# Performance work log

Measured on AMD Instinct MI355X. Metric: run time of the kernel, lower is better.

Reference implementation:

```python
import jax, jax.numpy as jnp
import numpy as np

B, T, V, D, H, L = 64, 256, 65, 384, 6, 6
HD = D // H
FF = 4 * D
EPS = 1e-5


def _layernorm(x, w, b):
    m = x.mean(-1, keepdims=True)
    v = ((x - m) ** 2).mean(-1, keepdims=True)
    return (x - m) / jnp.sqrt(v + EPS) * w + b


def setup_inputs() -> dict:
    key = jax.random.key(0)
    ks = jax.random.split(key, 20)
    s = lambda k, shape, scale=0.02: jax.random.normal(k, shape, dtype=jnp.float32) * scale
    inp = {
        'idx': jax.random.randint(ks[0], (B, T), 0, V),
        'tok_emb': s(ks[1], (V, D)),
        'pos_emb': s(ks[2], (T, D)),
        'ln1_w': jnp.ones((L, D), jnp.float32),
        'ln1_b': jnp.zeros((L, D), jnp.float32),
        'wq': s(ks[3], (L, H, D, HD)),
        'wk': s(ks[4], (L, H, D, HD)),
        'wv': s(ks[5], (L, H, D, HD)),
        'proj_w': s(ks[6], (L, D, D)),
        'proj_b': jnp.zeros((L, D), jnp.float32),
        'ln2_w': jnp.ones((L, D), jnp.float32),
        'ln2_b': jnp.zeros((L, D), jnp.float32),
        'ff_w1': s(ks[7], (L, D, FF)),
        'ff_b1': jnp.zeros((L, FF), jnp.float32),
        'ff_w2': s(ks[8], (L, FF, D)),
        'ff_b2': jnp.zeros((L, D), jnp.float32),
        'lnf_w': jnp.ones((D,), jnp.float32),
        'lnf_b': jnp.zeros((D,), jnp.float32),
        'head_w': s(ks[9], (D, V)),
        'head_b': jnp.zeros((V,), jnp.float32),
    }
    return inp


def reference(idx, tok_emb, pos_emb, ln1_w, ln1_b, wq, wk, wv, proj_w, proj_b,
              ln2_w, ln2_b, ff_w1, ff_b1, ff_w2, ff_b2, lnf_w, lnf_b, head_w, head_b):
    t = idx.shape[1]
    x = tok_emb[idx] + pos_emb[:t]  # [B,T,D]
    causal = jnp.tril(jnp.ones((t, t), bool))
    scale = D ** -0.5  # NOTE: original scales by n_embd**-0.5, not head_size
    for l in range(L):
        h = _layernorm(x, ln1_w[l], ln1_b[l])
        q = jnp.einsum('btd,hde->bhte', h, wq[l])
        k = jnp.einsum('btd,hde->bhte', h, wk[l])
        v = jnp.einsum('btd,hde->bhte', h, wv[l])
        wei = jnp.einsum('bhte,bhse->bhts', q, k) * scale
        wei = jnp.where(causal, wei, -jnp.inf)
        wei = jax.nn.softmax(wei, axis=-1)
        o = jnp.einsum('bhts,bhse->bhte', wei, v)
        o = o.transpose(0, 2, 1, 3).reshape(x.shape[0], t, D)  # concat heads
        x = x + o @ proj_w[l] + proj_b[l]
        h2 = _layernorm(x, ln2_w[l], ln2_b[l])
        x = x + jnp.maximum(h2 @ ff_w1[l] + ff_b1[l], 0.0) @ ff_w2[l] + ff_b2[l]
    x = _layernorm(x, lnf_w, lnf_b)
    logits = x @ head_w + head_b  # [B,T,V]
    return logits
```

## Files before the change

kernel.cpp:

```cpp
#include <hip/hip_runtime.h>
#include <hip/hip_bf16.h>
#include <math.h>

#define BB   64
#define TT   256
#define VV   65
#define DD   384
#define HH   6
#define HDD  64
#define LL   6
#define FFD  1536
#define BT   (BB * TT)
#define EPSL 1e-5f
#define SCALE 0.05103103630798287f

using bf16x8 = __attribute__((ext_vector_type(8))) short;
using f32x4  = __attribute__((ext_vector_type(4))) float;

__device__ __forceinline__ short f2bf(float f) {
    __hip_bfloat16 h = __float2bfloat16(f);
    return *reinterpret_cast<short*>(&h);
}

__device__ __forceinline__ void load_lds16(const void* g, void* lds_base) {
    __builtin_amdgcn_global_load_lds(
        (const __attribute__((address_space(1))) void*)g,
        (__attribute__((address_space(3))) void*)lds_base,
        16, 0, 0);
}

__global__ __launch_bounds__(256) void embed_k(const int* __restrict__ idx,
                                               const float* __restrict__ tok,
                                               const float* __restrict__ pos,
                                               float* __restrict__ x) {
    int i = blockIdx.x * 256 + threadIdx.x;
    int bt = i / 96;
    int d4 = i - bt * 96;
    int t  = bt & (TT - 1);
    float4 a = ((const float4*)tok)[(size_t)idx[bt] * 96 + d4];
    float4 p = ((const float4*)pos)[(size_t)t * 96 + d4];
    float4 o;
    o.x = a.x + p.x; o.y = a.y + p.y; o.z = a.z + p.z; o.w = a.w + p.w;
    ((float4*)x)[i] = o;
}

__global__ __launch_bounds__(256) void ln_k(const float* __restrict__ in,
                                            const float* __restrict__ w,
                                            const float* __restrict__ b,
                                            short* __restrict__ out) {
    int row  = blockIdx.x * 4 + (threadIdx.x >> 6);
    int lane = threadIdx.x & 63;
    const float* p = in + (size_t)row * DD;
    float vals[6];
    float s = 0.f;
#pragma unroll
    for (int j = 0; j < 6; ++j) { vals[j] = p[lane + 64 * j]; s += vals[j]; }
#pragma unroll
    for (int off = 32; off; off >>= 1) s += __shfl_xor(s, off);
    float mean = s * (1.0f / DD);
    float s2 = 0.f;
#pragma unroll
    for (int j = 0; j < 6; ++j) { float d = vals[j] - mean; s2 += d * d; }
#pragma unroll
    for (int off = 32; off; off >>= 1) s2 += __shfl_xor(s2, off);
    float rstd = rsqrtf(s2 * (1.0f / DD) + EPSL);
    short* po = out + (size_t)row * DD;
#pragma unroll
    for (int j = 0; j < 6; ++j) {
        int c = lane + 64 * j;
        po[c] = f2bf((vals[j] - mean) * rstd * w[c] + b[c]);
    }
}

__global__ __launch_bounds__(256) void wconv_k(const float* __restrict__ W,
                                               short* __restrict__ Wt,
                                               int K, int N, int Npad) {
    __shared__ float tile[32][33];
    W  += (size_t)blockIdx.z * K * N;
    Wt += (size_t)blockIdx.z * Npad * K;
    const int t  = threadIdx.x;
    const int c  = t & 31;
    const int r8 = t >> 5;
    const int k0 = blockIdx.y * 32;
    const int n0 = blockIdx.x * 32;
#pragma unroll
    for (int p = 0; p < 4; ++p) {
        int kk = r8 + 8 * p;
        int n  = n0 + c;
        tile[kk][c] = (n < N) ? W[(size_t)(k0 + kk) * N + n] : 0.f;
    }
    __syncthreads();
#pragma unroll
    for (int p = 0; p < 4; ++p) {
        int nl = r8 + 8 * p;
        Wt[(size_t)(n0 + nl) * K + k0 + c] = f2bf(tile[c][nl]);
    }
}

__global__ __launch_bounds__(256) void qkvconv_k(const float* __restrict__ wq,
                                                 const float* __restrict__ wk,
                                                 const float* __restrict__ wv,
                                                 short* __restrict__ Wt) {
    int tid = blockIdx.x * 256 + threadIdx.x;
    int e  = tid & 63;
    int k  = (tid >> 6) % 384;
    int r2 = (tid >> 6) / 384;
    int h  = r2 % 6;
    int r3 = r2 / 6;
    int part = r3 % 3;
    int l  = r3 / 3;
    const float* src = (part == 0) ? wq : (part == 1) ? wk : wv;
    float v = src[(((size_t)l * 6 + h) * 384 + k) * 64 + e];
    Wt[((size_t)l * 1152 + part * 384 + h * 64 + e) * 384 + k] = f2bf(v);
}

__global__ __launch_bounds__(512, 4) void gemm8_k(
    const short* __restrict__ A,
    const short* __restrict__ Bt,
    const float* __restrict__ bias,
    const float* __restrict__ res,
    float* __restrict__ out32,
    short* __restrict__ out16,
    int M, int K, int ldC, int ld16, int Nmax, int relu) {
    __shared__ short As[2][8192];
    __shared__ short Bs[2][8192];
    const int t  = threadIdx.x;
    const int w  = t >> 6;
    const int l  = t & 63;

    const int gx  = gridDim.x;
    const int nwg = gx * gridDim.y;
    const int lin = blockIdx.y * gx + blockIdx.x;
    const int cpx = nwg >> 3;
    const int swz = (lin & 7) * cpx + (lin >> 3);
    const int m0 = (swz / gx) * 128;
    const int n0 = (swz % gx) * 128;

    const int wr = w >> 2, wc = w & 3;
    const int fr = l & 15, fq = l >> 4;

    int srow[2], scol[2];
#pragma unroll
    for (int qi = 0; qi < 2; ++qi) {
        int S = (w * 2 + qi) * 1024 + l * 16;
        int r = S >> 7;
        int c = (S >> 4) & 7;
        srow[qi] = r;
        scol[qi] = c ^ (r & 7);
    }

    f32x4 acc[4][2];
#pragma unroll
    for (int i = 0; i < 4; ++i)
#pragma unroll
        for (int j = 0; j < 2; ++j) acc[i][j] = (f32x4)(0.0f);

    const int nt = K >> 6;
    int cur = 0;

#pragma unroll
    for (int qi = 0; qi < 2; ++qi) {
        load_lds16(A + (size_t)(m0 + srow[qi]) * K + scol[qi] * 8,
                   (char*)As[0] + (w * 2 + qi) * 1024);
        load_lds16(Bt + (size_t)(n0 + srow[qi]) * K + scol[qi] * 8,
                   (char*)Bs[0] + (w * 2 + qi) * 1024);
    }
    asm volatile("s_waitcnt vmcnt(0)" ::: "memory");
    __syncthreads();

    for (int tk = 0; tk < nt; ++tk) {
        const int k1 = (tk + 1) << 6;
        if (tk + 1 < nt) {
#pragma unroll
            for (int qi = 0; qi < 2; ++qi) {
                load_lds16(A + (size_t)(m0 + srow[qi]) * K + k1 + scol[qi] * 8,
                           (char*)As[cur ^ 1] + (w * 2 + qi) * 1024);
                load_lds16(Bt + (size_t)(n0 + srow[qi]) * K + k1 + scol[qi] * 8,
                           (char*)Bs[cur ^ 1] + (w * 2 + qi) * 1024);
            }
        }
        const char* Ab = (const char*)As[cur];
        const char* Bb = (const char*)Bs[cur];
#pragma unroll
        for (int ks = 0; ks < 2; ++ks) {
            const int kc = ks * 4 + fq;
            bf16x8 af[4], bfv[2];
#pragma unroll
            for (int mf = 0; mf < 4; ++mf) {
                int ar = wr * 64 + mf * 16 + fr;
                af[mf] = *reinterpret_cast<const bf16x8*>(
                    Ab + ar * 128 + ((kc ^ (ar & 7)) << 4));
            }
#pragma unroll
            for (int nf = 0; nf < 2; ++nf) {
                int br = wc * 32 + nf * 16 + fr;
                bfv[nf] = *reinterpret_cast<const bf16x8*>(
                    Bb + br * 128 + ((kc ^ (br & 7)) << 4));
            }
#pragma unroll
            for (int mf = 0; mf < 4; ++mf)
#pragma unroll
                for (int nf = 0; nf < 2; ++nf)
                    acc[mf][nf] = __builtin_amdgcn_mfma_f32_16x16x32_bf16(
                        af[mf], bfv[nf], acc[mf][nf], 0, 0, 0);
        }
        if (tk + 1 < nt) {
            asm volatile("s_waitcnt vmcnt(0)" ::: "memory");
            __syncthreads();
            cur ^= 1;
        }
    }

#pragma unroll
    for (int mf = 0; mf < 4; ++mf) {
#pragma unroll
        for (int nf = 0; nf < 2; ++nf) {
            int n = n0 + wc * 32 + nf * 16 + fr;
            if (n < Nmax) {
#pragma unroll
                for (int j = 0; j < 4; ++j) {
                    int m = m0 + wr * 64 + mf * 16 + fq * 4 + j;
                    float v = acc[mf][nf][j];
                    if (bias)  v += bias[n];
                    if (res)   v += res[(size_t)m * ldC + n];
                    if (relu)  v = fmaxf(v, 0.f);
                    if (out32) out32[(size_t)m * ldC + n] = v;
                    if (out16) out16[(size_t)m * ld16 + n] = f2bf(v);
                }
            }
        }
    }
}

__global__ __launch_bounds__(256) void attn_mfma_k(const short* __restrict__ qkv,
                                                   short* __restrict__ o) {
    __shared__ short Vt[16384];
    __shared__ short Pw[4][4096];

    const int hh = blockIdx.x;
    const int bb = blockIdx.y;
    const int t  = threadIdx.x;
    const int w  = t >> 6;
    const int lane = t & 63;
    const int fr = lane & 15, fq = lane >> 4;
    const int bt0 = bb * TT;

    {
        const int r0 = (t & 127) * 2;
        const int dbase = (t >> 7) * 32;
        const short* v0 = qkv + (size_t)(bt0 + r0) * 1152 + 768 + hh * 64 + dbase;
        short a0[32], a1[32];
#pragma unroll
        for (int i = 0; i < 4; ++i) {
            *(bf16x8*)(a0 + i * 8) = *(const bf16x8*)(v0 + i * 8);
            *(bf16x8*)(a1 + i * 8) = *(const bf16x8*)(v0 + 1152 + i * 8);
        }
#pragma unroll
        for (int i = 0; i < 32; ++i) {
            int d = dbase + i;
            int byte = (d * 512 + r0 * 2) ^ ((d & 7) << 4);
            unsigned int pk = (unsigned int)(unsigned short)a0[i] |
                              ((unsigned int)(unsigned short)a1[i] << 16);
            *(unsigned int*)((char*)Vt + byte) = pk;
        }
    }
    __syncthreads();

    char* PwW = (char*)Pw[w];

    bf16x8 qb[4][2];
#pragma unroll
    for (int nf = 0; nf < 4; ++nf)
#pragma unroll
        for (int ks = 0; ks < 2; ++ks)
            qb[nf][ks] = *(const bf16x8*)(qkv + (size_t)(bt0 + w * 64 + nf * 16 + fr) * 1152 +
                                          hh * 64 + ks * 32 + fq * 8);

    f32x4 o_acc[4][4];
#pragma unroll
    for (int i = 0; i < 4; ++i)
#pragma unroll
        for (int j = 0; j < 4; ++j) o_acc[i][j] = (f32x4)(0.0f);
    float m_run[4], l_run[4];
#pragma unroll
    for (int nf = 0; nf < 4; ++nf) { m_run[nf] = -1e30f; l_run[nf] = 0.f; }

    for (int kt = 0; kt <= w; ++kt) {
        bf16x8 ak[4][2];
#pragma unroll
        for (int mf = 0; mf < 4; ++mf)
#pragma unroll
            for (int ks = 0; ks < 2; ++ks)
                ak[mf][ks] = *(const bf16x8*)(qkv + (size_t)(bt0 + kt * 64 + mf * 16 + fr) * 1152 +
                                              384 + hh * 64 + ks * 32 + fq * 8);

        f32x4 s[4][4];
#pragma unroll
        for (int i = 0; i < 4; ++i)
#pragma unroll
            for (int j = 0; j < 4; ++j) s[i][j] = (f32x4)(0.0f);
#pragma unroll
        for (int ks = 0; ks < 2; ++ks)
#pragma unroll
            for (int mf = 0; mf < 4; ++mf)
#pragma unroll
                for (int nf = 0; nf < 4; ++nf)
                    s[mf][nf] = __builtin_amdgcn_mfma_f32_16x16x32_bf16(
                        ak[mf][ks], qb[nf][ks], s[mf][nf], 0, 0, 0);

        const bool diag = (kt == w);
#pragma unroll
        for (int mf = 0; mf < 4; ++mf)
#pragma unroll
            for (int nf = 0; nf < 4; ++nf)
#pragma unroll
                for (int j = 0; j < 4; ++j) {
                    float v = s[mf][nf][j] * SCALE;
                    if (diag && (mf * 16 + fq * 4 + j > nf * 16 + fr)) v = -1e30f;
                    s[mf][nf][j] = v;
                }

        float fac[4];
#pragma unroll
        for (int nf = 0; nf < 4; ++nf) {
            float mx = -1e30f;
#pragma unroll
            for (int mf = 0; mf < 4; ++mf)
#pragma unroll
                for (int j = 0; j < 4; ++j) mx = fmaxf(mx, s[mf][nf][j]);
            mx = fmaxf(mx, __shfl_xor(mx, 16));
            mx = fmaxf(mx, __shfl_xor(mx, 32));
            float mnew = fmaxf(m_run[nf], mx);
            fac[nf] = __expf(m_run[nf] - mnew);
            m_run[nf] = mnew;
        }

#pragma unroll
        for (int nf = 0; nf < 4; ++nf) {
            float ps = 0.f;
#pragma unroll
            for (int mf = 0; mf < 4; ++mf)
#pragma unroll
                for (int j = 0; j < 4; ++j) {
                    float p = __expf(s[mf][nf][j] - m_run[nf]);
                    s[mf][nf][j] = p;
                    ps += p;
                }
            ps += __shfl_xor(ps, 16);
            ps += __shfl_xor(ps, 32);
            l_run[nf] = l_run[nf] * fac[nf] + ps;
        }

#pragma unroll
        for (int mf = 0; mf < 4; ++mf)
#pragma unroll
            for (int nf = 0; nf < 4; ++nf) {
                unsigned long long pk =
                    (unsigned long long)(unsigned short)f2bf(s[mf][nf][0]) |
                    ((unsigned long long)(unsigned short)f2bf(s[mf][nf][1]) << 16) |
                    ((unsigned long long)(unsigned short)f2bf(s[mf][nf][2]) << 32) |
                    ((unsigned long long)(unsigned short)f2bf(s[mf][nf][3]) << 48);
                int q = nf * 16 + fr;
                int byte = (q * 128 + mf * 32 + fq * 8) ^ ((q & 7) << 4);
                *(unsigned long long*)(PwW + byte) = pk;
            }

#pragma unroll
        for (int j = 0; j < 4; ++j) {
            int src = (lane & 48) + ((lane & 48) >> 2) + j;
#pragma unroll
            for (int mo = 0; mo < 4; ++mo) {
                float f = __shfl(fac[mo], src);
#pragma unroll
                for (int df = 0; df < 4; ++df) o_acc[mo][df][j] *= f;
            }
        }

        bf16x8 ap[4][2], bv[4][2];
#pragma unroll
        for (int mo = 0; mo < 4; ++mo)
#pragma unroll
            for (int ks = 0; ks < 2; ++ks) {
                int byte = ((mo * 16 + fr) * 128 + ks * 64 + fq * 16) ^ ((fr & 7) << 4);
                ap[mo][ks] = *(const bf16x8*)(PwW + byte);
            }
#pragma unroll
        for (int df = 0; df < 4; ++df)
#pragma unroll
            for (int ks = 0; ks < 2; ++ks) {
                int byte = ((df * 16 + fr) * 512 + kt * 128 + ks * 64 + fq * 16) ^ ((fr & 7) << 4);
                bv[df][ks] = *(const bf16x8*)((const char*)Vt + byte);
            }
#pragma unroll
        for (int ks = 0; ks < 2; ++ks)
#pragma unroll
            for (int mo = 0; mo < 4; ++mo)
#pragma unroll
                for (int df = 0; df < 4; ++df)
                    o_acc[mo][df] = __builtin_amdgcn_mfma_f32_16x16x32_bf16(
                        ap[mo][ks], bv[df][ks], o_acc[mo][df], 0, 0, 0);
    }

    float linv[4];
#pragma unroll
    for (int nf = 0; nf < 4; ++nf) linv[nf] = 1.0f / l_run[nf];
#pragma unroll
    for (int j = 0; j < 4; ++j) {
        int src = (lane & 48) + ((lane & 48) >> 2) + j;
#pragma unroll
        for (int mo = 0; mo < 4; ++mo) {
            float li = __shfl(linv[mo], src);
#pragma unroll
            for (int df = 0; df < 4; ++df) {
                float val = o_acc[mo][df][j] * li;
                o[(size_t)(bt0 + w * 64 + mo * 16 + fq * 4 + j) * DD + hh * 64 + df * 16 + fr] =
                    f2bf(val);
            }
        }
    }
}

extern "C" void kernel_launch(void* const* d_in, const int* in_sizes, int n_in,
                              void* d_out, int out_size, void* d_ws, size_t ws_size,
                              hipStream_t stream) {
    const int*   idx     = (const int*)d_in[0];
    const float* tok_emb = (const float*)d_in[1];
    const float* pos_emb = (const float*)d_in[2];
    const float* ln1_w   = (const float*)d_in[3];
    const float* ln1_b   = (const float*)d_in[4];
    const float* wq      = (const float*)d_in[5];
    const float* wk      = (const float*)d_in[6];
    const float* wv      = (const float*)d_in[7];
    const float* proj_w  = (const float*)d_in[8];
    const float* proj_b  = (const float*)d_in[9];
    const float* ln2_w   = (const float*)d_in[10];
    const float* ln2_b   = (const float*)d_in[11];
    const float* ff_w1   = (const float*)d_in[12];
    const float* ff_b1   = (const float*)d_in[13];
    const float* ff_w2   = (const float*)d_in[14];
    const float* ff_b2   = (const float*)d_in[15];
    const float* lnf_w   = (const float*)d_in[16];
    const float* lnf_b   = (const float*)d_in[17];
    const float* head_w  = (const float*)d_in[18];
    const float* head_b  = (const float*)d_in[19];
    float* out = (float*)d_out;

    char* p = (char*)d_ws;
    float* x      = (float*)p;  p += (size_t)BT * DD * 4;
    short* qkv16  = (short*)p;  p += (size_t)BT * 1152 * 2;
    short* h16    = (short*)p;  p += (size_t)BT * DD * 2;
    short* o16    = (short*)p;  p += (size_t)BT * DD * 2;
    short* ff16   = (short*)p;  p += (size_t)BT * FFD * 2;
    short* wqkvT  = (short*)p;  p += (size_t)LL * 1152 * 384 * 2;
    short* projT  = (short*)p;  p += (size_t)LL * 384 * 384 * 2;
    short* ff1T   = (short*)p;  p += (size_t)LL * 1536 * 384 * 2;
    short* ff2T   = (short*)p;  p += (size_t)LL * 384 * 1536 * 2;
    short* headT  = (short*)p;  p += (size_t)128 * 384 * 2;

    const dim3 blk(256);
    const dim3 blk512(512);

    qkvconv_k<<<dim3(2654208 / 256), blk, 0, stream>>>(wq, wk, wv, wqkvT);
    wconv_k<<<dim3(12, 12, 6), blk, 0, stream>>>(proj_w, projT, 384, 384, 384);
    wconv_k<<<dim3(48, 12, 6), blk, 0, stream>>>(ff_w1, ff1T, 384, 1536, 1536);
    wconv_k<<<dim3(12, 48, 6), blk, 0, stream>>>(ff_w2, ff2T, 1536, 384, 384);
    wconv_k<<<dim3(4, 12, 1), blk, 0, stream>>>(head_w, headT, 384, 65, 128);

    embed_k<<<dim3((BT * 96) / 256), blk, 0, stream>>>(idx, tok_emb, pos_emb, x);

    const dim3 gLN(BT / 4);
    const dim3 gAttn(HH, BB);
    const dim3 gQKV(1152 / 128, BT / 128);
    const dim3 gD(384 / 128, BT / 128);
    const dim3 gFF(1536 / 128, BT / 128);
    const dim3 gHead(1, BT / 128);

    for (int l = 0; l < LL; ++l) {
        const size_t dOff = (size_t)l * DD;

        ln_k<<<gLN, blk, 0, stream>>>(x, ln1_w + dOff, ln1_b + dOff, h16);

        gemm8_k<<<gQKV, blk512, 0, stream>>>(h16, wqkvT + (size_t)l * 1152 * 384,
                                             nullptr, nullptr, nullptr, qkv16,
                                             BT, 384, 1152, 1152, 1152, 0);

        attn_mfma_k<<<gAttn, blk, 0, stream>>>(qkv16, o16);

        gemm8_k<<<gD, blk512, 0, stream>>>(o16, projT + (size_t)l * 384 * 384,
                                           proj_b + dOff, x, x, nullptr,
                                           BT, 384, 384, 0, 384, 0);

        ln_k<<<gLN, blk, 0, stream>>>(x, ln2_w + dOff, ln2_b + dOff, h16);

        gemm8_k<<<gFF, blk512, 0, stream>>>(h16, ff1T + (size_t)l * 1536 * 384,
                                            ff_b1 + (size_t)l * FFD, nullptr,
                                            nullptr, ff16,
                                            BT, 384, 1536, 1536, 1536, 1);

        gemm8_k<<<gD, blk512, 0, stream>>>(ff16, ff2T + (size_t)l * 384 * 1536,
                                           ff_b2 + dOff, x, x, nullptr,
                                           BT, 1536, 384, 0, 384, 0);
    }

    ln_k<<<gLN, blk, 0, stream>>>(x, lnf_w, lnf_b, h16);
    gemm8_k<<<gHead, blk512, 0, stream>>>(h16, headT, head_b, nullptr, out, nullptr,
                                          BT, 384, 65, 0, 65, 0);
}
```

Measured before the change: 1.368 ms.

## Replace LDS-staged GEMM with direct global-to-register fragment loads

The GEMM no longer stages A and B tiles through shared memory with global_load_lds and barriers. Each wave now loads its MFMA fragments straight from global memory into registers, double-buffered across two k-tiles. This removes LDS traffic and __syncthreads, but loses cross-wave reuse: each A row is fetched by 4 waves and each B row by 2, so global/L2 traffic rises, and the loads are 16-byte strided per row rather than fully coalesced. Register pressure also rises, and the occupancy hint in launch_bounds is dropped.

```diff
diff --git a/kernel.cpp b/kernel.cpp
--- a/kernel.cpp
+++ b/kernel.cpp
@@ -20,13 +20,6 @@
 __device__ __forceinline__ short f2bf(float f) {
     __hip_bfloat16 h = __float2bfloat16(f);
     return *reinterpret_cast<short*>(&h);
-}
-
-__device__ __forceinline__ void load_lds16(const void* g, void* lds_base) {
-    __builtin_amdgcn_global_load_lds(
-        (const __attribute__((address_space(1))) void*)g,
-        (__attribute__((address_space(3))) void*)lds_base,
-        16, 0, 0);
 }
 
 __global__ __launch_bounds__(256) void embed_k(const int* __restrict__ idx,
@@ -114,7 +107,7 @@
     Wt[((size_t)l * 1152 + part * 384 + h * 64 + e) * 384 + k] = f2bf(v);
 }
 
-__global__ __launch_bounds__(512, 4) void gemm8_k(
+__global__ __launch_bounds__(512) void gemmreg_k(
     const short* __restrict__ A,
     const short* __restrict__ Bt,
     const float* __restrict__ bias,
@@ -122,8 +115,6 @@
     float* __restrict__ out32,
     short* __restrict__ out16,
     int M, int K, int ldC, int ld16, int Nmax, int relu) {
-    __shared__ short As[2][8192];
-    __shared__ short Bs[2][8192];
     const int t  = threadIdx.x;
     const int w  = t >> 6;
     const int l  = t & 63;
@@ -139,15 +130,14 @@
     const int wr = w >> 2, wc = w & 3;
     const int fr = l & 15, fq = l >> 4;
 
-    int srow[2], scol[2];
-#pragma unroll
-    for (int qi = 0; qi < 2; ++qi) {
-        int S = (w * 2 + qi) * 1024 + l * 16;
-        int r = S >> 7;
-        int c = (S >> 4) & 7;
-        srow[qi] = r;
-        scol[qi] = c ^ (r & 7);
-    }
+    const short* Ap[4];
+#pragma unroll
+    for (int mf = 0; mf < 4; ++mf)
+        Ap[mf] = A + (size_t)(m0 + wr * 64 + mf * 16 + fr) * K + fq * 8;
+    const short* Bp[2];
+#pragma unroll
+    for (int nf = 0; nf < 2; ++nf)
+        Bp[nf] = Bt + (size_t)(n0 + wc * 32 + nf * 16 + fr) * K + fq * 8;
 
     f32x4 acc[4][2];
 #pragma unroll
@@ -156,59 +146,64 @@
         for (int j = 0; j < 2; ++j) acc[i][j] = (f32x4)(0.0f);
 
     const int nt = K >> 6;
-    int cur = 0;
-
-#pragma unroll
-    for (int qi = 0; qi < 2; ++qi) {
-        load_lds16(A + (size_t)(m0 + srow[qi]) * K + scol[qi] * 8,
-                   (char*)As[0] + (w * 2 + qi) * 1024);
-        load_lds16(Bt + (size_t)(n0 + srow[qi]) * K + scol[qi] * 8,
-                   (char*)Bs[0] + (w * 2 + qi) * 1024);
-    }
-    asm volatile("s_waitcnt vmcnt(0)" ::: "memory");
-    __syncthreads();
-
-    for (int tk = 0; tk < nt; ++tk) {
-        const int k1 = (tk + 1) << 6;
-        if (tk + 1 < nt) {
-#pragma unroll
-            for (int qi = 0; qi < 2; ++qi) {
-                load_lds16(A + (size_t)(m0 + srow[qi]) * K + k1 + scol[qi] * 8,
-                           (char*)As[cur ^ 1] + (w * 2 + qi) * 1024);
-                load_lds16(Bt + (size_t)(n0 + srow[qi]) * K + k1 + scol[qi] * 8,
-                           (char*)Bs[cur ^ 1] + (w * 2 + qi) * 1024);
-            }
-        }
-        const char* Ab = (const char*)As[cur];
-        const char* Bb = (const char*)Bs[cur];
-#pragma unroll
-        for (int ks = 0; ks < 2; ++ks) {
-            const int kc = ks * 4 + fq;
-            bf16x8 af[4], bfv[2];
-#pragma unroll
-            for (int mf = 0; mf < 4; ++mf) {
-                int ar = wr * 64 + mf * 16 + fr;
-                af[mf] = *reinterpret_cast<const bf16x8*>(
-                    Ab + ar * 128 + ((kc ^ (ar & 7)) << 4));
-            }
-#pragma unroll
-            for (int nf = 0; nf < 2; ++nf) {
-                int br = wc * 32 + nf * 16 + fr;
-                bfv[nf] = *reinterpret_cast<const bf16x8*>(
-                    Bb + br * 128 + ((kc ^ (br & 7)) << 4));
-            }
+
+    bf16x8 a0[4][2], b0[2][2], a1[4][2], b1[2][2];
+
+#pragma unroll
+    for (int mf = 0; mf < 4; ++mf)
+#pragma unroll
+        for (int ks = 0; ks < 2; ++ks)
+            a0[mf][ks] = *(const bf16x8*)(Ap[mf] + ks * 32);
+#pragma unroll
+    for (int nf = 0; nf < 2; ++nf)
+#pragma unroll
+        for (int ks = 0; ks < 2; ++ks)
+            b0[nf][ks] = *(const bf16x8*)(Bp[nf] + ks * 32);
+
+    for (int tk = 0; tk < nt; tk += 2) {
+        const int kb = (tk + 1) << 6;
+#pragma unroll
+        for (int mf = 0; mf < 4; ++mf)
+#pragma unroll
+            for (int ks = 0; ks < 2; ++ks)
+                a1[mf][ks] = *(const bf16x8*)(Ap[mf] + kb + ks * 32);
+#pragma unroll
+        for (int nf = 0; nf < 2; ++nf)
+#pragma unroll
+            for (int ks = 0; ks < 2; ++ks)
+                b1[nf][ks] = *(const bf16x8*)(Bp[nf] + kb + ks * 32);
+
+#pragma unroll
+        for (int ks = 0; ks < 2; ++ks)
 #pragma unroll
             for (int mf = 0; mf < 4; ++mf)
 #pragma unroll
                 for (int nf = 0; nf < 2; ++nf)
                     acc[mf][nf] = __builtin_amdgcn_mfma_f32_16x16x32_bf16(
-                        af[mf], bfv[nf], acc[mf][nf], 0, 0, 0);
-        }
-        if (tk + 1 < nt) {
-            asm volatile("s_waitcnt vmcnt(0)" ::: "memory");
-            __syncthreads();
-            cur ^= 1;
-        }
+                        a0[mf][ks], b0[nf][ks], acc[mf][nf], 0, 0, 0);
+
+        if (tk + 2 < nt) {
+            const int kc = (tk + 2) << 6;
+#pragma unroll
+            for (int mf = 0; mf < 4; ++mf)
+#pragma unroll
+                for (int ks = 0; ks < 2; ++ks)
+                    a0[mf][ks] = *(const bf16x8*)(Ap[mf] + kc + ks * 32);
+#pragma unroll
+            for (int nf = 0; nf < 2; ++nf)
+#pragma unroll
+                for (int ks = 0; ks < 2; ++ks)
+                    b0[nf][ks] = *(const bf16x8*)(Bp[nf] + kc + ks * 32);
+        }
+
+#pragma unroll
+        for (int ks = 0; ks < 2; ++ks)
+#pragma unroll
+            for (int mf = 0; mf < 4; ++mf)
+#pragma unroll
+                for (int nf = 0; nf < 2; ++nf)
+                    acc[mf][nf] = __builtin_amdgcn_mfma_f32_16x16x32_bf16(
+                        a1[mf][ks], b1[nf][ks], acc[mf][nf], 0, 0, 0);
     }
 
 #pragma unroll
@@ -480,29 +475,29 @@
 
         ln_k<<<gLN, blk, 0, stream>>>(x, ln1_w + dOff, ln1_b + dOff, h16);
 
-        gemm8_k<<<gQKV, blk512, 0, stream>>>(h16, wqkvT + (size_t)l * 1152 * 384,
-                                             nullptr, nullptr, nullptr, qkv16,
-                                             BT, 384, 1152, 1152, 1152, 0);
+        gemmreg_k<<<gQKV, blk512, 0, stream>>>(h16, wqkvT + (size_t)l * 1152 * 384,
+                                               nullptr, nullptr, nullptr, qkv16,
+                                               BT, 384, 1152, 1152, 1152, 0);
 
         attn_mfma_k<<<gAttn, blk, 0, stream>>>(qkv16, o16);
 
-        gemm8_k<<<gD, blk512, 0, stream>>>(o16, projT + (size_t)l * 384 * 384,
-                                           proj_b + dOff, x, x, nullptr,
-                                           BT, 384, 384, 0, 384, 0);
+        gemmreg_k<<<gD, blk512, 0, stream>>>(o16, projT + (size_t)l * 384 * 384,
+                                             proj_b + dOff, x, x, nullptr,
+                                             BT, 384, 384, 0, 384, 0);
 
         ln_k<<<gLN, blk, 0, stream>>>(x, ln2_w + dOff, ln2_b + dOff, h16);
 
-        gemm8_k<<<gFF, blk512, 0, stream>>>(h16, ff1T + (size_t)l * 1536 * 384,
-                                            ff_b1 + (size_t)l * FFD, nullptr,
-                                            nullptr, ff16,
-                                            BT, 384, 1536, 1536, 1536, 1);
-
-        gemm8_k<<<gD, blk512, 0, stream>>>(ff16, ff2T + (size_t)l * 384 * 1536,
-                                           ff_b2 + dOff, x, x, nullptr,
-                                           BT, 1536, 384, 0, 384, 0);
+        gemmreg_k<<<gFF, blk512, 0, stream>>>(h16, ff1T + (size_t)l * 1536 * 384,
+                                              ff_b1 + (size_t)l * FFD, nullptr,
+                                              nullptr, ff16,
+                                              BT, 384, 1536, 1536, 1536, 1);
+
+        gemmreg_k<<<gD, blk512, 0, stream>>>(ff16, ff2T + (size_t)l * 384 * 1536,
+                                             ff_b2 + dOff, x, x, nullptr,
+                                             BT, 1536, 384, 0, 384, 0);
     }
 
     ln_k<<<gLN, blk, 0, stream>>>(x, lnf_w, lnf_b, h16);
-    gemm8_k<<<gHead, blk512, 0, stream>>>(h16, headT, head_b, nullptr, out, nullptr,
-                                          BT, 384, 65, 0, 65, 0);
-}
+    gemmreg_k<<<gHead, blk512, 0, stream>>>(h16, headT, head_b, nullptr, out, nullptr,
+                                            BT, 384, 65, 0, 65, 0);
+}
```

Measured after the change: 3.124 ms. 128% more time.

## Switch GEMMs to 64x64 tiles with single-buffered LDS and more blocks

Applied to the files above, without the earlier changes.

Replaces the 128x128, 512-thread double-buffered GEMM with a 64x64, 256-thread single-buffered kernel. Grids grow fourfold so each launch has more workgroups across the CUs, and the kernel adds s_setprio around the MFMA section. The trade is the loss of global-load/compute overlap from double buffering, and lower operand reuse per tile, which means more global traffic.

```diff
diff --git a/kernel.cpp b/kernel.cpp
--- a/kernel.cpp
+++ b/kernel.cpp
@@ -114,7 +114,7 @@
     Wt[((size_t)l * 1152 + part * 384 + h * 64 + e) * 384 + k] = f2bf(v);
 }
 
-__global__ __launch_bounds__(512, 4) void gemm8_k(
+__global__ __launch_bounds__(256, 8) void gemm64_k(
     const short* __restrict__ A,
     const short* __restrict__ Bt,
     const float* __restrict__ bias,
@@ -122,8 +122,8 @@
     float* __restrict__ out32,
     short* __restrict__ out16,
     int M, int K, int ldC, int ld16, int Nmax, int relu) {
-    __shared__ short As[2][8192];
-    __shared__ short Bs[2][8192];
+    __shared__ short As[4096];
+    __shared__ short Bs[4096];
     const int t  = threadIdx.x;
     const int w  = t >> 6;
     const int l  = t & 63;
@@ -133,93 +133,82 @@
     const int lin = blockIdx.y * gx + blockIdx.x;
     const int cpx = nwg >> 3;
     const int swz = (lin & 7) * cpx + (lin >> 3);
-    const int m0 = (swz / gx) * 128;
-    const int n0 = (swz % gx) * 128;
-
-    const int wr = w >> 2, wc = w & 3;
+    const int m0 = (swz / gx) * 64;
+    const int n0 = (swz % gx) * 64;
+
+    const int wr = w >> 1, wc = w & 1;
     const int fr = l & 15, fq = l >> 4;
 
     int srow[2], scol[2];
 #pragma unroll
     for (int qi = 0; qi < 2; ++qi) {
-        int S = (w * 2 + qi) * 1024 + l * 16;
-        int r = S >> 7;
-        int c = (S >> 4) & 7;
+        int s = w * 2 + qi;
+        int r = s * 8 + (l >> 3);
+        int c = l & 7;
         srow[qi] = r;
         scol[qi] = c ^ (r & 7);
     }
 
-    f32x4 acc[4][2];
-#pragma unroll
-    for (int i = 0; i < 4; ++i)
+    f32x4 acc[2][2];
+#pragma unroll
+    for (int i = 0; i < 2; ++i)
 #pragma unroll
         for (int j = 0; j < 2; ++j) acc[i][j] = (f32x4)(0.0f);
 
     const int nt = K >> 6;
-    int cur = 0;
-
-#pragma unroll
-    for (int qi = 0; qi < 2; ++qi) {
-        load_lds16(A + (size_t)(m0 + srow[qi]) * K + scol[qi] * 8,
-                   (char*)As[0] + (w * 2 + qi) * 1024);
-        load_lds16(Bt + (size_t)(n0 + srow[qi]) * K + scol[qi] * 8,
-                   (char*)Bs[0] + (w * 2 + qi) * 1024);
-    }
-    asm volatile("s_waitcnt vmcnt(0)" ::: "memory");
-    __syncthreads();
 
     for (int tk = 0; tk < nt; ++tk) {
-        const int k1 = (tk + 1) << 6;
-        if (tk + 1 < nt) {
-#pragma unroll
-            for (int qi = 0; qi < 2; ++qi) {
-                load_lds16(A + (size_t)(m0 + srow[qi]) * K + k1 + scol[qi] * 8,
-                           (char*)As[cur ^ 1] + (w * 2 + qi) * 1024);
-                load_lds16(Bt + (size_t)(n0 + srow[qi]) * K + k1 + scol[qi] * 8,
-                           (char*)Bs[cur ^ 1] + (w * 2 + qi) * 1024);
-            }
-        }
-        const char* Ab = (const char*)As[cur];
-        const char* Bb = (const char*)Bs[cur];
+        const int k0 = tk << 6;
+#pragma unroll
+        for (int qi = 0; qi < 2; ++qi) {
+            load_lds16(A + (size_t)(m0 + srow[qi]) * K + k0 + scol[qi] * 8,
+                       (char*)As + (w * 2 + qi) * 1024);
+        }
+#pragma unroll
+        for (int qi = 0; qi < 2; ++qi) {
+            load_lds16(Bt + (size_t)(n0 + srow[qi]) * K + k0 + scol[qi] * 8,
+                       (char*)Bs + (w * 2 + qi) * 1024);
+        }
+        asm volatile("s_waitcnt vmcnt(0)" ::: "memory");
+        __syncthreads();
+
+        __builtin_amdgcn_s_setprio(1);
 #pragma unroll
         for (int ks = 0; ks < 2; ++ks) {
             const int kc = ks * 4 + fq;
-            bf16x8 af[4], bfv[2];
-#pragma unroll
-            for (int mf = 0; mf < 4; ++mf) {
-                int ar = wr * 64 + mf * 16 + fr;
+            bf16x8 af[2], bfv[2];
+#pragma unroll
+            for (int mf = 0; mf < 2; ++mf) {
+                int ar = wr * 32 + mf * 16 + fr;
                 af[mf] = *reinterpret_cast<const bf16x8*>(
-                    Ab + ar * 128 + ((kc ^ (ar & 7)) << 4));
+                    (const char*)As + ar * 128 + ((kc ^ (ar & 7)) << 4));
             }
 #pragma unroll
             for (int nf = 0; nf < 2; ++nf) {
                 int br = wc * 32 + nf * 16 + fr;
                 bfv[nf] = *reinterpret_cast<const bf16x8*>(
-                    Bb + br * 128 + ((kc ^ (br & 7)) << 4));
-            }
-#pragma unroll
-            for (int mf = 0; mf < 4; ++mf)
+                    (const char*)Bs + br * 128 + ((kc ^ (br & 7)) << 4));
+            }
+#pragma unroll
+            for (int mf = 0; mf < 2; ++mf)
 #pragma unroll
                 for (int nf = 0; nf < 2; ++nf)
                     acc[mf][nf] = __builtin_amdgcn_mfma_f32_16x16x32_bf16(
                         af[mf], bfv[nf], acc[mf][nf], 0, 0, 0);
         }
-        if (tk + 1 < nt) {
-            asm volatile("s_waitcnt vmcnt(0)" ::: "memory");
-            __syncthreads();
-            cur ^= 1;
-        }
-    }
-
-#pragma unroll
-    for (int mf = 0; mf < 4; ++mf) {
+        __builtin_amdgcn_s_setprio(0);
+        __syncthreads();
+    }
+
+#pragma unroll
+    for (int mf = 0; mf < 2; ++mf) {
 #pragma unroll
         for (int nf = 0; nf < 2; ++nf) {
             int n = n0 + wc * 32 + nf * 16 + fr;
             if (n < Nmax) {
 #pragma unroll
                 for (int j = 0; j < 4; ++j) {
-                    int m = m0 + wr * 64 + mf * 16 + fq * 4 + j;
+                    int m = m0 + wr * 32 + mf * 16 + fq * 4 + j;
                     float v = acc[mf][nf][j];
                     if (bias)  v += bias[n];
                     if (res)   v += res[(size_t)m * ldC + n];
@@ -458,7 +447,6 @@
     short* headT  = (short*)p;  p += (size_t)128 * 384 * 2;
 
     const dim3 blk(256);
-    const dim3 blk512(512);
 
     qkvconv_k<<<dim3(2654208 / 256), blk, 0, stream>>>(wq, wk, wv, wqkvT);
     wconv_k<<<dim3(12, 12, 6), blk, 0, stream>>>(proj_w, projT, 384, 384, 384);
@@ -470,39 +458,39 @@
 
     const dim3 gLN(BT / 4);
     const dim3 gAttn(HH, BB);
-    const dim3 gQKV(1152 / 128, BT / 128);
-    const dim3 gD(384 / 128, BT / 128);
-    const dim3 gFF(1536 / 128, BT / 128);
-    const dim3 gHead(1, BT / 128);
+    const dim3 gQKV(1152 / 64, BT / 64);
+    const dim3 gD(384 / 64, BT / 64);
+    const dim3 gFF(1536 / 64, BT / 64);
+    const dim3 gHead(128 / 64, BT / 64);
 
     for (int l = 0; l < LL; ++l) {
         const size_t dOff = (size_t)l * DD;
 
         ln_k<<<gLN, blk, 0, stream>>>(x, ln1_w + dOff, ln1_b + dOff, h16);
 
-        gemm8_k<<<gQKV, blk512, 0, stream>>>(h16, wqkvT + (size_t)l * 1152 * 384,
-                                             nullptr, nullptr, nullptr, qkv16,
-                                             BT, 384, 1152, 1152, 1152, 0);
+        gemm64_k<<<gQKV, blk, 0, stream>>>(h16, wqkvT + (size_t)l * 1152 * 384,
+                                           nullptr, nullptr, nullptr, qkv16,
+                                           BT, 384, 1152, 1152, 1152, 0);
 
         attn_mfma_k<<<gAttn, blk, 0, stream>>>(qkv16, o16);
 
-        gemm8_k<<<gD, blk512, 0, stream>>>(o16, projT + (size_t)l * 384 * 384,
-                                           proj_b + dOff, x, x, nullptr,
-                                           BT, 384, 384, 0, 384, 0);
+        gemm64_k<<<gD, blk, 0, stream>>>(o16, projT + (size_t)l * 384 * 384,
+                                         proj_b + dOff, x, x, nullptr,
+                                         BT, 384, 384, 0, 384, 0);
 
         ln_k<<<gLN, blk, 0, stream>>>(x, ln2_w + dOff, ln2_b + dOff, h16);
 
-        gemm8_k<<<gFF, blk512, 0, stream>>>(h16, ff1T + (size_t)l * 1536 * 384,
-                                            ff_b1 + (size_t)l * FFD, nullptr,
-                                            nullptr, ff16,
-                                            BT, 384, 1536, 1536, 1536, 1);
-
-        gemm8_k<<<gD, blk512, 0, stream>>>(ff16, ff2T + (size_t)l * 384 * 1536,
-                                           ff_b2 + dOff, x, x, nullptr,
-                                           BT, 1536, 384, 0, 384, 0);
+        gemm64_k<<<gFF, blk, 0, stream>>>(h16, ff1T + (size_t)l * 1536 * 384,
+                                          ff_b1 + (size_t)l * FFD, nullptr,
+                                          nullptr, ff16,
+                                          BT, 384, 1536, 1536, 1536, 1);
+
+        gemm64_k<<<gD, blk, 0, stream>>>(ff16, ff2T + (size_t)l * 384 * 1536,
+                                         ff_b2 + dOff, x, x, nullptr,
+                                         BT, 1536, 384, 0, 384, 0);
     }
 
     ln_k<<<gLN, blk, 0, stream>>>(x, lnf_w, lnf_b, h16);
-    gemm8_k<<<gHead, blk512, 0, stream>>>(h16, headT, head_b, nullptr, out, nullptr,
-                                          BT, 384, 65, 0, 65, 0);
-}
+    gemm64_k<<<gHead, blk, 0, stream>>>(h16, headT, head_b, nullptr, out, nullptr,
+                                        BT, 384, 65, 0, 65, 0);
+}
```

New measurement: 1.195 ms. 12.6% less time.
